# Optimization experiments

Measured on AMD Instinct MI355X. Metric: run time of the kernel, lower is better.

The kernel has to match this reference:

```python
import jax, jax.numpy as jnp
import numpy as np

ENC2 = 1024   # encoder_hidden_dim * 2
DEC = 1024    # decoder_hidden_dim
ATT = 512     # attention_dim
B, S = 32, 2048


def setup_inputs() -> dict:
    key = jax.random.key(0)
    ks = jax.random.split(key, 7)
    sW = 1.0 / np.sqrt(DEC)
    sU = 1.0 / np.sqrt(ENC2)
    sv = 1.0 / np.sqrt(ATT)
    return {
        "decoder_hidden": jax.random.normal(ks[0], (B, DEC), jnp.float32),
        "encoder_all_hidden": jax.random.normal(ks[1], (B, S, ENC2), jnp.float32),
        "W_w": jax.random.uniform(ks[2], (DEC, ATT), jnp.float32, -sW, sW),
        "W_b": jax.random.uniform(ks[3], (ATT,), jnp.float32, -sW, sW),
        "U_w": jax.random.uniform(ks[4], (ENC2, ATT), jnp.float32, -sU, sU),
        "U_b": jax.random.uniform(ks[5], (ATT,), jnp.float32, -sU, sU),
        "v_w": jax.random.uniform(ks[6], (ATT, 1), jnp.float32, -sv, sv),
    }


def reference(decoder_hidden, encoder_all_hidden, W_w, W_b, U_w, U_b, v_w):
    # Ws: (B, 1, A); Uh: (B, S, A)
    Ws = (decoder_hidden @ W_w + W_b)[:, None, :]
    Uh = jnp.einsum('bse,ea->bsa', encoder_all_hidden, U_w) + U_b
    energy = jnp.einsum('bsa,ao->bs', jnp.tanh(Ws + Uh), v_w)
    alpha = jax.nn.softmax(energy, axis=1)
    return alpha
```

## Files before the change

kernel.cpp:

```cpp
#include <hip/hip_runtime.h>
#include <hip/hip_bf16.h>
#include <math.h>

#define ENC2 1024
#define DECD 1024
#define ATT 512
#define NBATCH 32
#define SEQ 2048
#define MTOT (NBATCH*SEQ)

#define BM 128
#define BN2 256
#define BK 32
#define LDK 40

typedef __attribute__((ext_vector_type(8))) short short8;
typedef __attribute__((ext_vector_type(4))) short short4v;
typedef __attribute__((ext_vector_type(4))) float f32x4;

static __device__ __forceinline__ unsigned pk2(float a, float b) {
  __hip_bfloat162 h = __float22bfloat162_rn(float2{a, b});
  union { __hip_bfloat162 h; unsigned u; } c; c.h = h;
  return c.u;
}

static __device__ __forceinline__ float fast_tanh(float x) {
  float ax = fabsf(x);
  float e = __expf(2.f * ax);
  float t = 1.f - 2.f / (e + 1.f);
  return copysignf(t, x);
}

__global__ __launch_bounds__(512) void prep_kernel(
    const float* __restrict__ U_w, short* __restrict__ U_wT,
    const float* __restrict__ dh, const float* __restrict__ W_w,
    const float* __restrict__ W_b, const float* __restrict__ U_b,
    float* __restrict__ Wsb) {
  __shared__ float tile[64][65];
  __shared__ float dsh[DECD];
  __shared__ float part[4][128];
  const int t = threadIdx.x;

  if (blockIdx.x < 128) {
    const int kt = blockIdx.x >> 3;
    const int ct = blockIdx.x & 7;
    const int k0 = kt * 64, c0 = ct * 64;
    const int r = t >> 3, cc = (t & 7) * 8;
    float4 v0 = *(const float4*)(U_w + (size_t)(k0 + r) * ATT + c0 + cc);
    float4 v1 = *(const float4*)(U_w + (size_t)(k0 + r) * ATT + c0 + cc + 4);
    tile[r][cc+0] = v0.x; tile[r][cc+1] = v0.y; tile[r][cc+2] = v0.z; tile[r][cc+3] = v0.w;
    tile[r][cc+4] = v1.x; tile[r][cc+5] = v1.y; tile[r][cc+6] = v1.z; tile[r][cc+7] = v1.w;
    __syncthreads();
    const int c = t >> 3, kk = (t & 7) * 8;
    union { short8 s; unsigned u[4]; } o;
    o.u[0] = pk2(tile[kk+0][c], tile[kk+1][c]);
    o.u[1] = pk2(tile[kk+2][c], tile[kk+3][c]);
    o.u[2] = pk2(tile[kk+4][c], tile[kk+5][c]);
    o.u[3] = pk2(tile[kk+6][c], tile[kk+7][c]);
    *(short8*)(U_wT + (size_t)(c0 + c) * ENC2 + k0 + kk) = o.s;
  } else {
    const int bid = blockIdx.x - 128;
    const int b  = bid >> 2;
    const int a0 = (bid & 3) * 128;
    for (int i = t; i < DECD; i += 512) dsh[i] = dh[(size_t)b * DECD + i];
    __syncthreads();
    const int ks = t >> 7;
    const int a  = t & 127;
    const float* wp = W_w + (size_t)(ks * 256) * ATT + a0 + a;
    float s0 = 0.f, s1 = 0.f, s2 = 0.f, s3 = 0.f;
    #pragma unroll 4
    for (int kk = 0; kk < 256; kk += 4) {
      s0 = fmaf(dsh[ks*256 + kk + 0], wp[(size_t)(kk + 0) * ATT], s0);
      s1 = fmaf(dsh[ks*256 + kk + 1], wp[(size_t)(kk + 1) * ATT], s1);
      s2 = fmaf(dsh[ks*256 + kk + 2], wp[(size_t)(kk + 2) * ATT], s2);
      s3 = fmaf(dsh[ks*256 + kk + 3], wp[(size_t)(kk + 3) * ATT], s3);
    }
    part[ks][a] = (s0 + s1) + (s2 + s3);
    __syncthreads();
    if (t < 128) {
      float v = part[0][t] + part[1][t] + part[2][t] + part[3][t];
      Wsb[(size_t)b * ATT + a0 + t] = v + W_b[a0 + t] + U_b[a0 + t];
    }
  }
}

__global__ __launch_bounds__(512) void energy_kernel(
    const float* __restrict__ A,
    const short* __restrict__ Bt,
    const float* __restrict__ Wsb,
    const float* __restrict__ vw,
    float* __restrict__ epart)
{
  __shared__ __align__(16) short As[2][BM * LDK];
  __shared__ __align__(16) short Bs[2][BN2 * LDK];
  __shared__ float eps[4][BM];

  const int tid = threadIdx.x;
  const int bid = blockIdx.x;
  const int mt = (bid >> 4) * 8 + (bid & 7);
  const int nt = (bid >> 3) & 1;
  const int row0 = mt * BM;
  const int col0 = nt * BN2;
  const int bidx = row0 / SEQ;

  const int lane = tid & 63;
  const int wid  = tid >> 6;
  const int wm   = wid >> 2;
  const int wn   = wid & 3;

  const int ar = tid >> 2, ak = (tid & 3) * 8;
  const int bc = tid >> 1, bk = (tid & 1) * 16;

  const int fr = lane & 15;
  const int k0 = (lane >> 4) * 8;

  f32x4 acc[4][4];
  #pragma unroll
  for (int m = 0; m < 4; m++)
    #pragma unroll
    for (int n = 0; n < 4; n++) acc[m][n] = (f32x4){0.f, 0.f, 0.f, 0.f};

  const float* Abase = A + (size_t)row0 * ENC2;
  const short* Bbase = Bt + (size_t)col0 * ENC2;

  float4 aR0, aR1;
  short8 bR0, bR1;

  aR0 = *(const float4*)(Abase + (size_t)ar * ENC2 + ak);
  aR1 = *(const float4*)(Abase + (size_t)ar * ENC2 + ak + 4);
  bR0 = *(const short8*)(Bbase + (size_t)bc * ENC2 + bk);
  bR1 = *(const short8*)(Bbase + (size_t)bc * ENC2 + bk + 8);
  {
    union { short8 s; unsigned u[4]; } w;
    w.u[0] = pk2(aR0.x, aR0.y); w.u[1] = pk2(aR0.z, aR0.w);
    w.u[2] = pk2(aR1.x, aR1.y); w.u[3] = pk2(aR1.z, aR1.w);
    *(short8*)(&As[0][ar * LDK + ak]) = w.s;
    *(short8*)(&Bs[0][bc * LDK + bk]) = bR0;
    *(short8*)(&Bs[0][bc * LDK + bk + 8]) = bR1;
  }
  __syncthreads();

  const int NT = ENC2 / BK;
  for (int kt = 0; kt < NT; kt++) {
    const int cur = kt & 1;
    const bool more = (kt + 1 < NT);
    if (more) {
      const float* Ab = Abase + (kt + 1) * BK;
      aR0 = *(const float4*)(Ab + (size_t)ar * ENC2 + ak);
      aR1 = *(const float4*)(Ab + (size_t)ar * ENC2 + ak + 4);
      const short* Bb = Bbase + (kt + 1) * BK;
      bR0 = *(const short8*)(Bb + (size_t)bc * ENC2 + bk);
      bR1 = *(const short8*)(Bb + (size_t)bc * ENC2 + bk + 8);
    }
    short8 af[4], bfr[4];
    #pragma unroll
    for (int m = 0; m < 4; m++)
      af[m] = *(const short8*)(&As[cur][(wm*64 + m*16 + fr) * LDK + k0]);
    #pragma unroll
    for (int n = 0; n < 4; n++)
      bfr[n] = *(const short8*)(&Bs[cur][(wn*64 + n*16 + fr) * LDK + k0]);
    #pragma unroll
    for (int m = 0; m < 4; m++)
      #pragma unroll
      for (int n = 0; n < 4; n++)
        acc[m][n] = __builtin_amdgcn_mfma_f32_16x16x32_bf16(af[m], bfr[n], acc[m][n], 0, 0, 0);
    if (more) {
      union { short8 s; unsigned u[4]; } w;
      w.u[0] = pk2(aR0.x, aR0.y); w.u[1] = pk2(aR0.z, aR0.w);
      w.u[2] = pk2(aR1.x, aR1.y); w.u[3] = pk2(aR1.z, aR1.w);
      *(short8*)(&As[cur ^ 1][ar * LDK + ak]) = w.s;
      *(short8*)(&Bs[cur ^ 1][bc * LDK + bk]) = bR0;
      *(short8*)(&Bs[cur ^ 1][bc * LDK + bk + 8]) = bR1;
    }
    __syncthreads();
  }

  float vv[4], wsb[4];
  #pragma unroll
  for (int n = 0; n < 4; n++) {
    const int gc = col0 + wn*64 + n*16 + fr;
    vv[n]  = vw[gc];
    wsb[n] = Wsb[(size_t)bidx * ATT + gc];
  }
  const int rg = lane >> 4;
  #pragma unroll
  for (int m = 0; m < 4; m++) {
    float part[4] = {0.f, 0.f, 0.f, 0.f};
    #pragma unroll
    for (int n = 0; n < 4; n++) {
      #pragma unroll
      for (int r = 0; r < 4; r++)
        part[r] += vv[n] * fast_tanh(acc[m][n][r] + wsb[n]);
    }
    #pragma unroll
    for (int r = 0; r < 4; r++) {
      float p = part[r];
      p += __shfl_xor(p, 1);
      p += __shfl_xor(p, 2);
      p += __shfl_xor(p, 4);
      p += __shfl_xor(p, 8);
      if (fr == 0) eps[wn][wm*64 + m*16 + rg*4 + r] = p;
    }
  }
  __syncthreads();
  if (tid < BM) {
    float s = eps[0][tid] + eps[1][tid] + eps[2][tid] + eps[3][tid];
    epart[(size_t)nt * MTOT + row0 + tid] = s;
  }
}

__global__ __launch_bounds__(512) void softmax_kernel(const float* __restrict__ epart,
                                                      float* __restrict__ out) {
  __shared__ float redmax[8];
  __shared__ float redsum[8];
  const int b = blockIdx.x, t = threadIdx.x;
  const float* e0 = epart + (size_t)b * SEQ;
  const float* e1 = epart + (size_t)MTOT + (size_t)b * SEQ;
  float vals[4];
  float mx = -1e30f;
  #pragma unroll
  for (int i = 0; i < 4; i++) {
    vals[i] = e0[t + i*512] + e1[t + i*512];
    mx = fmaxf(mx, vals[i]);
  }
  #pragma unroll
  for (int off = 1; off < 64; off <<= 1) mx = fmaxf(mx, __shfl_xor(mx, off));
  if ((t & 63) == 0) redmax[t >> 6] = mx;
  __syncthreads();
  mx = redmax[0];
  #pragma unroll
  for (int i = 1; i < 8; i++) mx = fmaxf(mx, redmax[i]);
  float sum = 0.f;
  #pragma unroll
  for (int i = 0; i < 4; i++) { vals[i] = expf(vals[i] - mx); sum += vals[i]; }
  #pragma unroll
  for (int off = 1; off < 64; off <<= 1) sum += __shfl_xor(sum, off);
  if ((t & 63) == 0) redsum[t >> 6] = sum;
  __syncthreads();
  float tot = 0.f;
  #pragma unroll
  for (int i = 0; i < 8; i++) tot += redsum[i];
  const float inv = 1.f / tot;
  #pragma unroll
  for (int i = 0; i < 4; i++) out[(size_t)b * SEQ + t + i*512] = vals[i] * inv;
}

extern "C" void kernel_launch(void* const* d_in, const int* in_sizes, int n_in,
                              void* d_out, int out_size, void* d_ws, size_t ws_size,
                              hipStream_t stream) {
  const float* dh  = (const float*)d_in[0];
  const float* enc = (const float*)d_in[1];
  const float* W_w = (const float*)d_in[2];
  const float* W_b = (const float*)d_in[3];
  const float* U_w = (const float*)d_in[4];
  const float* U_b = (const float*)d_in[5];
  const float* v_w = (const float*)d_in[6];
  float* out = (float*)d_out;

  char* ws = (char*)d_ws;
  float* epart = (float*)ws;
  float* Wsb   = (float*)(ws + 512 * 1024);
  short* U_wT  = (short*)(ws + 576 * 1024);

  prep_kernel<<<256, 512, 0, stream>>>(U_w, U_wT, dh, W_w, W_b, U_b, Wsb);
  energy_kernel<<<1024, 512, 0, stream>>>(enc, U_wT, Wsb, v_w, epart);
  softmax_kernel<<<NBATCH, 512, 0, stream>>>(epart, out);
}
```

Before: 131.0 us.

## Stream GEMM tiles via direct global-to-LDS loads with deeper multi-stage pipeline

Replaces register-staged global loads plus LDS stores with global_load_lds direct DMA into shared memory. The fp32 encoder tile is kept as fp32 in LDS and converted to bf16 at fragment-read time. The K loop is restructured into 64-wide double buffers split into two halves, with vmcnt-based fences, and s_setprio is raised around the MFMA bursts. The aim is to hide global latency and free VGPRs from the staging path, at the cost of doubled LDS footprint for A (fp32) and possible bank conflicts, since the padded layout is gone.

Measured after the change: 256.4 us. 1.96x slower.

```diff
diff --git a/kernel.cpp b/kernel.cpp
--- a/kernel.cpp
+++ b/kernel.cpp
@@ -11,8 +11,7 @@
 
 #define BM 128
 #define BN2 256
-#define BK 32
-#define LDK 40
+#define BK 64
 
 typedef __attribute__((ext_vector_type(8))) short short8;
 typedef __attribute__((ext_vector_type(4))) short short4v;
@@ -29,6 +28,12 @@
   float e = __expf(2.f * ax);
   float t = 1.f - 2.f / (e + 1.f);
   return copysignf(t, x);
+}
+
+static __device__ __forceinline__ void gload_lds16(const void* g, void* l) {
+  __builtin_amdgcn_global_load_lds(
+      (const __attribute__((address_space(1))) void*)g,
+      (__attribute__((address_space(3))) void*)l, 16, 0, 0);
 }
 
 __global__ __launch_bounds__(512) void prep_kernel(
@@ -84,6 +89,42 @@
   }
 }
 
+
+#define STAGE(BUF, H, CB)                                                      \
+  do {                                                                         \
+    gload_lds16(aS + (CB),          &As[BUF][H][w*512]);                       \
+    gload_lds16(aS + (CB) + 4,      &As[BUF][H][w*512 + 256]);                 \
+    gload_lds16(bS0 + (CB),         &Bs[BUF][H][w*1024]);                      \
+    gload_lds16(bS1 + (CB),         &Bs[BUF][H][w*1024 + 512]);                \
+  } while (0)
+
+#define COMPUTE(C, H)                                                          \
+  do {                                                                         \
+    short8 bf0 = *(const short8*)(&Bs[C][H][bB + 0*512]);                      \
+    short8 bf1 = *(const short8*)(&Bs[C][H][bB + 1*512]);                      \
+    short8 bf2 = *(const short8*)(&Bs[C][H][bB + 2*512]);                      \
+    short8 bf3 = *(const short8*)(&Bs[C][H][bB + 3*512]);                      \
+    __builtin_amdgcn_s_setprio(1);                                             \
+    _Pragma("unroll")                                                          \
+    for (int m = 0; m < 4; m++) {                                              \
+      const float* ap = &As[C][H][aB + m*512];                                 \
+      float4 x0 = *(const float4*)ap;                                          \
+      float4 x1 = *(const float4*)(ap + 256);                                  \
+      union { short8 s; unsigned u[4]; } aw;                                   \
+      aw.u[0] = pk2(x0.x, x0.y); aw.u[1] = pk2(x0.z, x0.w);                    \
+      aw.u[2] = pk2(x1.x, x1.y); aw.u[3] = pk2(x1.z, x1.w);                    \
+      acc[m][0] = __builtin_amdgcn_mfma_f32_16x16x32_bf16(aw.s, bf0, acc[m][0], 0, 0, 0); \
+      acc[m][1] = __builtin_amdgcn_mfma_f32_16x16x32_bf16(aw.s, bf1, acc[m][1], 0, 0, 0); \
+      acc[m][2] = __builtin_amdgcn_mfma_f32_16x16x32_bf16(aw.s, bf2, acc[m][2], 0, 0, 0); \
+      acc[m][3] = __builtin_amdgcn_mfma_f32_16x16x32_bf16(aw.s, bf3, acc[m][3], 0, 0, 0); \
+    }                                                                          \
+    __builtin_amdgcn_s_setprio(0);                                             \
+  } while (0)
+
+#define FENCE(VM)                                                              \
+  asm volatile("s_waitcnt vmcnt(" VM ")" ::: "memory");                        \
+  __builtin_amdgcn_s_barrier();
+
 __global__ __launch_bounds__(512) void energy_kernel(
     const float* __restrict__ A,
     const short* __restrict__ Bt,
@@ -91,9 +132,8 @@
     const float* __restrict__ vw,
     float* __restrict__ epart)
 {
-  __shared__ __align__(16) short As[2][BM * LDK];
-  __shared__ __align__(16) short Bs[2][BN2 * LDK];
-  __shared__ float eps[4][BM];
+  __shared__ __align__(16) float As[2][2][4096];
+  __shared__ __align__(16) short Bs[2][2][8192];
 
   const int tid = threadIdx.x;
   const int bid = blockIdx.x;
@@ -104,15 +144,18 @@
   const int bidx = row0 / SEQ;
 
   const int lane = tid & 63;
-  const int wid  = tid >> 6;
-  const int wm   = wid >> 2;
-  const int wn   = wid & 3;
-
-  const int ar = tid >> 2, ak = (tid & 3) * 8;
-  const int bc = tid >> 1, bk = (tid & 1) * 16;
-
-  const int fr = lane & 15;
-  const int k0 = (lane >> 4) * 8;
+  const int w    = tid >> 6;
+  const int wm   = w >> 2;
+  const int wn   = w & 3;
+  const int fr   = lane & 15;
+  const int kh   = lane >> 4;
+
+  const int aB = wm*2048 + kh*64 + fr*4;
+  const int bB = wn*2048 + kh*128 + fr*8;
+
+  const float* aS  = A  + (size_t)(row0 + w*16 + (lane & 15)) * ENC2 + (lane >> 4) * 8;
+  const short* bS0 = Bt + (size_t)(col0 + (2*w + 0)*16 + (lane & 15)) * ENC2 + (lane >> 4) * 8;
+  const short* bS1 = Bt + (size_t)(col0 + (2*w + 1)*16 + (lane & 15)) * ENC2 + (lane >> 4) * 8;
 
   f32x4 acc[4][4];
   #pragma unroll
@@ -120,61 +163,30 @@
     #pragma unroll
     for (int n = 0; n < 4; n++) acc[m][n] = (f32x4){0.f, 0.f, 0.f, 0.f};
 
-  const float* Abase = A + (size_t)row0 * ENC2;
-  const short* Bbase = Bt + (size_t)col0 * ENC2;
-
-  float4 aR0, aR1;
-  short8 bR0, bR1;
-
-  aR0 = *(const float4*)(Abase + (size_t)ar * ENC2 + ak);
-  aR1 = *(const float4*)(Abase + (size_t)ar * ENC2 + ak + 4);
-  bR0 = *(const short8*)(Bbase + (size_t)bc * ENC2 + bk);
-  bR1 = *(const short8*)(Bbase + (size_t)bc * ENC2 + bk + 8);
-  {
-    union { short8 s; unsigned u[4]; } w;
-    w.u[0] = pk2(aR0.x, aR0.y); w.u[1] = pk2(aR0.z, aR0.w);
-    w.u[2] = pk2(aR1.x, aR1.y); w.u[3] = pk2(aR1.z, aR1.w);
-    *(short8*)(&As[0][ar * LDK + ak]) = w.s;
-    *(short8*)(&Bs[0][bc * LDK + bk]) = bR0;
-    *(short8*)(&Bs[0][bc * LDK + bk + 8]) = bR1;
-  }
-  __syncthreads();
-
-  const int NT = ENC2 / BK;
-  for (int kt = 0; kt < NT; kt++) {
-    const int cur = kt & 1;
-    const bool more = (kt + 1 < NT);
-    if (more) {
-      const float* Ab = Abase + (kt + 1) * BK;
-      aR0 = *(const float4*)(Ab + (size_t)ar * ENC2 + ak);
-      aR1 = *(const float4*)(Ab + (size_t)ar * ENC2 + ak + 4);
-      const short* Bb = Bbase + (kt + 1) * BK;
-      bR0 = *(const short8*)(Bb + (size_t)bc * ENC2 + bk);
-      bR1 = *(const short8*)(Bb + (size_t)bc * ENC2 + bk + 8);
-    }
-    short8 af[4], bfr[4];
-    #pragma unroll
-    for (int m = 0; m < 4; m++)
-      af[m] = *(const short8*)(&As[cur][(wm*64 + m*16 + fr) * LDK + k0]);
-    #pragma unroll
-    for (int n = 0; n < 4; n++)
-      bfr[n] = *(const short8*)(&Bs[cur][(wn*64 + n*16 + fr) * LDK + k0]);
-    #pragma unroll
-    for (int m = 0; m < 4; m++)
-      #pragma unroll
-      for (int n = 0; n < 4; n++)
-        acc[m][n] = __builtin_amdgcn_mfma_f32_16x16x32_bf16(af[m], bfr[n], acc[m][n], 0, 0, 0);
-    if (more) {
-      union { short8 s; unsigned u[4]; } w;
-      w.u[0] = pk2(aR0.x, aR0.y); w.u[1] = pk2(aR0.z, aR0.w);
-      w.u[2] = pk2(aR1.x, aR1.y); w.u[3] = pk2(aR1.z, aR1.w);
-      *(short8*)(&As[cur ^ 1][ar * LDK + ak]) = w.s;
-      *(short8*)(&Bs[cur ^ 1][bc * LDK + bk]) = bR0;
-      *(short8*)(&Bs[cur ^ 1][bc * LDK + bk + 8]) = bR1;
-    }
-    __syncthreads();
-  }
-
+  STAGE(0, 0, 0);
+  STAGE(0, 1, 32);
+  STAGE(1, 0, 64);
+  FENCE("8");
+
+  for (int t = 0; t < 14; t++) {
+    const int c = t & 1;
+    STAGE(c ^ 1, 1, (t + 1) * 64 + 32);
+    COMPUTE(c, 0);
+    FENCE("8");
+    STAGE(c, 0, (t + 2) * 64);
+    COMPUTE(c, 1);
+    FENCE("8");
+  }
+  STAGE(1, 1, 15 * 64 + 32);
+  COMPUTE(0, 0);
+  FENCE("8");
+  COMPUTE(0, 1);
+  FENCE("4");
+  COMPUTE(1, 0);
+  FENCE("0");
+  COMPUTE(1, 1);
+
+  float* eps = (float*)&As[0][0][0];
   float vv[4], wsb[4];
   #pragma unroll
   for (int n = 0; n < 4; n++) {
@@ -199,12 +211,12 @@
       p += __shfl_xor(p, 2);
       p += __shfl_xor(p, 4);
       p += __shfl_xor(p, 8);
-      if (fr == 0) eps[wn][wm*64 + m*16 + rg*4 + r] = p;
+      if (fr == 0) eps[wn*BM + wm*64 + m*16 + rg*4 + r] = p;
     }
   }
   __syncthreads();
   if (tid < BM) {
-    float s = eps[0][tid] + eps[1][tid] + eps[2][tid] + eps[3][tid];
+    float s = eps[0*BM + tid] + eps[1*BM + tid] + eps[2*BM + tid] + eps[3*BM + tid];
     epart[(size_t)nt * MTOT + row0 + tid] = s;
   }
 }
```

## Fuse softmax into energy kernel using per-batch last-block atomic counter

Applied to the files above, without the earlier changes.

Drops the separate softmax launch. Each energy block publishes its partial energies and increments a per-batch atomic counter. The 32nd block to finish for a batch then runs the softmax for that batch. This removes one kernel launch and the tail gap between launches, but adds a memset, fences and atomics, and the final softmax for each batch runs serialized in its last block.

New measurement: 351.8 us. +168.5%, slower.

```diff
diff --git a/kernel.cpp b/kernel.cpp
--- a/kernel.cpp
+++ b/kernel.cpp
@@ -89,11 +89,15 @@
     const short* __restrict__ Bt,
     const float* __restrict__ Wsb,
     const float* __restrict__ vw,
-    float* __restrict__ epart)
+    float* __restrict__ epart,
+    unsigned* __restrict__ cnt,
+    float* __restrict__ out)
 {
   __shared__ __align__(16) short As[2][BM * LDK];
   __shared__ __align__(16) short Bs[2][BN2 * LDK];
   __shared__ float eps[4][BM];
+  __shared__ float redm[8], reds[8];
+  __shared__ unsigned sflag;
 
   const int tid = threadIdx.x;
   const int bid = blockIdx.x;
@@ -205,44 +209,51 @@
   __syncthreads();
   if (tid < BM) {
     float s = eps[0][tid] + eps[1][tid] + eps[2][tid] + eps[3][tid];
-    epart[(size_t)nt * MTOT + row0 + tid] = s;
-  }
-}
-
-__global__ __launch_bounds__(512) void softmax_kernel(const float* __restrict__ epart,
-                                                      float* __restrict__ out) {
-  __shared__ float redmax[8];
-  __shared__ float redsum[8];
-  const int b = blockIdx.x, t = threadIdx.x;
-  const float* e0 = epart + (size_t)b * SEQ;
-  const float* e1 = epart + (size_t)MTOT + (size_t)b * SEQ;
+    __hip_atomic_store(&epart[(size_t)nt * MTOT + row0 + tid], s,
+                       __ATOMIC_RELAXED, __HIP_MEMORY_SCOPE_AGENT);
+  }
+
+  __threadfence();
+  __syncthreads();
+  if (tid == 0) {
+    unsigned old = __hip_atomic_fetch_add(&cnt[bidx], 1u,
+                                          __ATOMIC_ACQ_REL, __HIP_MEMORY_SCOPE_AGENT);
+    sflag = (old == 31u);
+  }
+  __syncthreads();
+  if (!sflag) return;
+
+  const float* e0 = epart + (size_t)bidx * SEQ;
+  const float* e1 = epart + (size_t)MTOT + (size_t)bidx * SEQ;
   float vals[4];
   float mx = -1e30f;
   #pragma unroll
   for (int i = 0; i < 4; i++) {
-    vals[i] = e0[t + i*512] + e1[t + i*512];
+    float a0 = __hip_atomic_load(&e0[tid + i*512], __ATOMIC_RELAXED, __HIP_MEMORY_SCOPE_AGENT);
+    float a1 = __hip_atomic_load(&e1[tid + i*512], __ATOMIC_RELAXED, __HIP_MEMORY_SCOPE_AGENT);
+    vals[i] = a0 + a1;
     mx = fmaxf(mx, vals[i]);
   }
   #pragma unroll
   for (int off = 1; off < 64; off <<= 1) mx = fmaxf(mx, __shfl_xor(mx, off));
-  if ((t & 63) == 0) redmax[t >> 6] = mx;
-  __syncthreads();
-  mx = redmax[0];
-  #pragma unroll
-  for (int i = 1; i < 8; i++) mx = fmaxf(mx, redmax[i]);
+  if ((tid & 63) == 0) redm[tid >> 6] = mx;
+  __syncthreads();
+  mx = redm[0];
+  #pragma unroll
+  for (int i = 1; i < 8; i++) mx = fmaxf(mx, redm[i]);
   float sum = 0.f;
   #pragma unroll
   for (int i = 0; i < 4; i++) { vals[i] = expf(vals[i] - mx); sum += vals[i]; }
   #pragma unroll
   for (int off = 1; off < 64; off <<= 1) sum += __shfl_xor(sum, off);
-  if ((t & 63) == 0) redsum[t >> 6] = sum;
+  if ((tid & 63) == 0) reds[tid >> 6] = sum;
   __syncthreads();
   float tot = 0.f;
   #pragma unroll
-  for (int i = 0; i < 8; i++) tot += redsum[i];
+  for (int i = 0; i < 8; i++) tot += reds[i];
   const float inv = 1.f / tot;
   #pragma unroll
-  for (int i = 0; i < 4; i++) out[(size_t)b * SEQ + t + i*512] = vals[i] * inv;
+  for (int i = 0; i < 4; i++) out[(size_t)bidx * SEQ + tid + i*512] = vals[i] * inv;
 }
 
 extern "C" void kernel_launch(void* const* d_in, const int* in_sizes, int n_in,
@@ -258,11 +269,12 @@
   float* out = (float*)d_out;
 
   char* ws = (char*)d_ws;
-  float* epart = (float*)ws;
-  float* Wsb   = (float*)(ws + 512 * 1024);
-  short* U_wT  = (short*)(ws + 576 * 1024);
-
+  float*    epart = (float*)ws;
+  float*    Wsb   = (float*)(ws + 512 * 1024);
+  short*    U_wT  = (short*)(ws + 576 * 1024);
+  unsigned* cnt   = (unsigned*)(ws + 576 * 1024 + 1024 * 1024);
+
+  hipMemsetAsync(cnt, 0, NBATCH * sizeof(unsigned), stream);
   prep_kernel<<<256, 512, 0, stream>>>(U_w, U_wT, dh, W_w, W_b, U_b, Wsb);
-  energy_kernel<<<1024, 512, 0, stream>>>(enc, U_wT, Wsb, v_w, epart);
-  softmax_kernel<<<NBATCH, 512, 0, stream>>>(epart, out);
-}
+  energy_kernel<<<1024, 512, 0, stream>>>(enc, U_wT, Wsb, v_w, epart, cnt, out);
+}
```
